# Kernel optimization log

Measured on AMD Instinct MI355X. Metric: run time of the kernel, lower is better.

## Reference

```python
import jax, jax.numpy as jnp
import numpy as np
import math

# dims: batch, seq_len, d_model, heads, head_dim
B, L, DM, H, DH = 1, 4096, 1024, 16, 64
BS, W, MAXD, DFF = 64, 16, 256, 4096  # block_size, band width (blocks), max rel distance, ffn dim
NB = L // BS


def _static_layout():
    # Static block-sparse causal band layout: tgt block n attends to src blocks [n-W+1 .. n].
    # Mirrors construct_blocksparse_rel_ids: rel = tgt_pos - src_pos, pos ids start at 1
    # (0 reserved for padding), clamp rel<-1 -> -1, rel>max_distance -> max_distance, then +1.
    n = np.arange(NB)[:, None, None, None]
    w = np.arange(W)[None, :, None, None]
    i = np.arange(BS)[None, None, :, None]
    j = np.arange(BS)[None, None, None, :]
    src_blk = n - (W - 1) + w
    # valid: block exists; diagonal block (w==W-1) is causal within-block (j<=i)
    valid = (src_blk >= 0) & ((w < W - 1) | (j <= i))
    tgt_pos = n * BS + i + 1
    src_pos = np.clip(src_blk, 0, None) * BS + j + 1
    rel = np.clip(tgt_pos - src_pos, -1, MAXD) + 1
    rel = np.where(valid, rel, 0)  # masked positions get rel id 0 (as in masked_fill_)
    src_idx = np.clip(np.arange(NB)[:, None] - (W - 1) + np.arange(W)[None, :], 0, None)
    return jnp.asarray(rel), jnp.asarray(valid), jnp.asarray(src_idx)

REL_IDS, VALID, SRC_IDX = _static_layout()  # [NB,W,BS,BS], [NB,W,BS,BS], [NB,W]


def _ln(x, g, b):
    m = x.mean(-1, keepdims=True)
    v = ((x - m) ** 2).mean(-1, keepdims=True)
    return (x - m) * jax.lax.rsqrt(v + 1e-5) * g + b


def setup_inputs() -> dict:
    key = jax.random.key(0)
    ks = jax.random.split(key, 10)
    p = lambda k, shape: jax.random.normal(k, shape, jnp.float32) * 0.02
    return dict(
        x=jax.random.normal(ks[0], (B, L, DM), jnp.float32),
        Wq=p(ks[1], (DM, DM)), Wk=p(ks[2], (DM, DM)), Wv=p(ks[3], (DM, DM)),
        Wo=p(ks[4], (DM, DM)),
        rel_emb=p(ks[5], (MAXD + 2, H)),  # per-head relative position bias table
        ln1_g=jnp.ones((DM,), jnp.float32), ln1_b=jnp.zeros((DM,), jnp.float32),
        ln2_g=jnp.ones((DM,), jnp.float32), ln2_b=jnp.zeros((DM,), jnp.float32),
        W1=p(ks[6], (DM, DFF)), b1=jnp.zeros((DFF,), jnp.float32),
        W2=p(ks[7], (DFF, DM)), b2=jnp.zeros((DM,), jnp.float32),
    )


def reference(x, Wq, Wk, Wv, Wo, rel_emb, ln1_g, ln1_b, ln2_g, ln2_b, W1, b1, W2, b2):
    h = _ln(x, ln1_g, ln1_b)

    def heads(Wt):
        return (h @ Wt).reshape(B, NB, BS, H, DH).transpose(0, 3, 1, 2, 4)  # [B,H,NB,BS,DH]

    q, k, v = heads(Wq), heads(Wk), heads(Wv)
    k_band = k[:, :, SRC_IDX]  # gather nonzero src blocks -> [B,H,NB,W,BS,DH]
    v_band = v[:, :, SRC_IDX]
    scores = jnp.einsum('bhnid,bhnwjd->bhniwj', q, k_band) / math.sqrt(DH)
    # relative position bias, per block pair and head
    bias = rel_emb[REL_IDS].transpose(4, 0, 2, 1, 3)  # [H,NB,BS,W,BS]
    scores = scores + bias[None]
    mask = VALID.transpose(0, 2, 1, 3)  # [NB,BS,W,BS]
    scores = jnp.where(mask, scores, jnp.float32(-1e30))
    p = jax.nn.softmax(scores.reshape(B, H, NB, BS, W * BS), axis=-1)
    p = p.reshape(B, H, NB, BS, W, BS)
    o = jnp.einsum('bhniwj,bhnwjd->bhnid', p, v_band)
    o = o.transpose(0, 2, 3, 1, 4).reshape(B, L, DM) @ Wo
    x = x + o
    h2 = _ln(x, ln2_g, ln2_b)
    x = x + (jax.nn.gelu(h2 @ W1 + b1) @ W2 + b2)
    return x
```

## Files before the change

kernel.cpp:

```cpp
#include <hip/hip_runtime.h>
#include <math.h>

typedef __bf16 bf16x8 __attribute__((ext_vector_type(8)));
typedef short  s16x4  __attribute__((ext_vector_type(4)));
typedef float  f32x4  __attribute__((ext_vector_type(4)));
typedef short  s16x8  __attribute__((ext_vector_type(8)));

__device__ __forceinline__ unsigned short f2bf(float f) {
    unsigned int u = __float_as_uint(f);
    u += 0x7fffu + ((u >> 16) & 1u);
    return (unsigned short)(u >> 16);
}

__device__ __forceinline__ unsigned cvt_pk_bf16(float a, float b) {
    unsigned r;
    asm volatile("v_cvt_pk_bf16_f32 %0, %1, %2" : "=v"(r) : "v"(a), "v"(b));
    return r;
}

__device__ __forceinline__ f32x4 mfma16(s16x4 a, s16x4 b, f32x4 c) {
#if __has_builtin(__builtin_amdgcn_mfma_f32_16x16x16bf16_1k)
    return __builtin_amdgcn_mfma_f32_16x16x16bf16_1k(a, b, c, 0, 0, 0);
#else
    asm volatile("s_nop 3\n\t"
                 "v_mfma_f32_16x16x16_bf16 %0, %1, %2, %0\n\t"
                 "s_nop 7\n\t"
                 "s_nop 7"
                 : "+v"(c) : "v"(a), "v"(b));
    return c;
#endif
}

__device__ __forceinline__ float gelu_tanh(float x) {
    float x3 = x * x * x;
    float t = tanhf(0.7978845608028654f * (x + 0.044715f * x3));
    return 0.5f * x * (1.0f + t);
}

__global__ __launch_bounds__(256) void tcvt4_kernel(const float* __restrict__ p0,
                                                    const float* __restrict__ p1,
                                                    const float* __restrict__ p2,
                                                    const float* __restrict__ p3,
                                                    unsigned short* __restrict__ out) {
    __shared__ float tile[32][33];
    int z = blockIdx.z;
    const float* in = (z == 0) ? p0 : (z == 1) ? p1 : (z == 2) ? p2 : p3;
    unsigned short* o = out + (size_t)z * 1048576;
    int tx = threadIdx.x, ty = threadIdx.y;
    int k0 = blockIdx.y * 32, n0 = blockIdx.x * 32;
#pragma unroll
    for (int s = 0; s < 4; ++s)
        tile[ty + s * 8][tx] = in[(size_t)(k0 + ty + s * 8) * 1024 + n0 + tx];
    __syncthreads();
#pragma unroll
    for (int s = 0; s < 4; ++s)
        o[(size_t)(n0 + ty + s * 8) * 1024 + k0 + tx] = f2bf(tile[tx][ty + s * 8]);
}

__global__ __launch_bounds__(256) void tcvt_kernel(const float* __restrict__ in,
                                                   unsigned short* __restrict__ out,
                                                   int K, int N) {
    __shared__ float tile[32][33];
    int tx = threadIdx.x, ty = threadIdx.y;
    int k0 = blockIdx.y * 32, n0 = blockIdx.x * 32;
#pragma unroll
    for (int s = 0; s < 4; ++s)
        tile[ty + s * 8][tx] = in[(size_t)(k0 + ty + s * 8) * N + n0 + tx];
    __syncthreads();
#pragma unroll
    for (int s = 0; s < 4; ++s)
        out[(size_t)(n0 + ty + s * 8) * K + k0 + tx] = f2bf(tile[tx][ty + s * 8]);
}

__global__ __launch_bounds__(256) void ln_kernel(const float* __restrict__ x,
                                                 const float* __restrict__ g,
                                                 const float* __restrict__ b,
                                                 unsigned short* __restrict__ out) {
    int row = blockIdx.x;
    int tid = threadIdx.x;
    float4 v = ((const float4*)(x + (size_t)row * 1024))[tid];
    float s  = v.x + v.y + v.z + v.w;
    float ss = v.x * v.x + v.y * v.y + v.z * v.z + v.w * v.w;
#pragma unroll
    for (int o = 32; o > 0; o >>= 1) { s += __shfl_down(s, o); ss += __shfl_down(ss, o); }
    __shared__ float red[8];
    if ((tid & 63) == 0) { red[(tid >> 6) * 2] = s; red[(tid >> 6) * 2 + 1] = ss; }
    __syncthreads();
    s  = red[0] + red[2] + red[4] + red[6];
    ss = red[1] + red[3] + red[5] + red[7];
    float mean = s * (1.0f / 1024.0f);
    float var  = ss * (1.0f / 1024.0f) - mean * mean;
    float rs   = rsqrtf(var + 1e-5f);
    float4 gv = ((const float4*)g)[tid];
    float4 bv = ((const float4*)b)[tid];
    ushort4 o4;
    o4.x = f2bf((v.x - mean) * rs * gv.x + bv.x);
    o4.y = f2bf((v.y - mean) * rs * gv.y + bv.y);
    o4.z = f2bf((v.z - mean) * rs * gv.z + bv.z);
    o4.w = f2bf((v.w - mean) * rs * gv.w + bv.w);
    ((ushort4*)(out + (size_t)row * 1024))[tid] = o4;
}

__global__ __launch_bounds__(256) void reduceln_kernel(const unsigned short* __restrict__ part,
                                                       const float* __restrict__ xin,
                                                       const float* __restrict__ g,
                                                       const float* __restrict__ b,
                                                       float* __restrict__ x2,
                                                       unsigned short* __restrict__ outbf) {
    int row = blockIdx.x;
    int tid = threadIdx.x;
    int i4  = row * 256 + tid;
    float4 r = ((const float4*)xin)[i4];
    float v0 = r.x, v1 = r.y, v2 = r.z, v3 = r.w;
#pragma unroll
    for (int sl = 0; sl < 4; ++sl) {
        ushort4 u = ((const ushort4*)(part + (size_t)sl * 4194304))[i4];
        v0 += __uint_as_float((unsigned)u.x << 16);
        v1 += __uint_as_float((unsigned)u.y << 16);
        v2 += __uint_as_float((unsigned)u.z << 16);
        v3 += __uint_as_float((unsigned)u.w << 16);
    }
    float4 o; o.x = v0; o.y = v1; o.z = v2; o.w = v3;
    ((float4*)x2)[i4] = o;

    float s  = v0 + v1 + v2 + v3;
    float ss = v0 * v0 + v1 * v1 + v2 * v2 + v3 * v3;
#pragma unroll
    for (int off = 32; off > 0; off >>= 1) { s += __shfl_down(s, off); ss += __shfl_down(ss, off); }
    __shared__ float red[8];
    if ((tid & 63) == 0) { red[(tid >> 6) * 2] = s; red[(tid >> 6) * 2 + 1] = ss; }
    __syncthreads();
    s  = red[0] + red[2] + red[4] + red[6];
    ss = red[1] + red[3] + red[5] + red[7];
    float mean = s * (1.0f / 1024.0f);
    float var  = ss * (1.0f / 1024.0f) - mean * mean;
    float rs   = rsqrtf(var + 1e-5f);
    float4 gv = ((const float4*)g)[tid];
    float4 bv = ((const float4*)b)[tid];
    ushort4 o4;
    o4.x = f2bf((v0 - mean) * rs * gv.x + bv.x);
    o4.y = f2bf((v1 - mean) * rs * gv.y + bv.y);
    o4.z = f2bf((v2 - mean) * rs * gv.z + bv.z);
    o4.w = f2bf((v3 - mean) * rs * gv.w + bv.w);
    ((ushort4*)(outbf + (size_t)row * 1024))[tid] = o4;
}

__global__ __launch_bounds__(256) void tvt_kernel(const unsigned short* __restrict__ in,
                                                  unsigned short* __restrict__ out) {
    __shared__ unsigned short tile[64][72];
    int t = threadIdx.x;
    int l0 = blockIdx.x * 64, c0 = blockIdx.y * 64;
    int tr = t >> 3, tc = (t & 7) * 8;
#pragma unroll
    for (int s = 0; s < 2; ++s) {
        int r = tr + s * 32;
        s16x8 v = *(const s16x8*)(in + (size_t)(l0 + r) * 3072 + 2048 + c0 + tc);
        *(s16x8*)(&tile[r][tc]) = v;
    }
    __syncthreads();
#pragma unroll
    for (int s = 0; s < 2; ++s) {
        int c = tr + s * 32;
        s16x8 w;
#pragma unroll
        for (int e = 0; e < 8; ++e) w[e] = (short)tile[tc + e][c];
        *(s16x8*)(out + (size_t)(c0 + c) * 4096 + l0 + tc) = w;
    }
}

__device__ __forceinline__ void stage8(const unsigned short* __restrict__ src_row0, int ld,
                                       unsigned short* ldsdst, int lane) {
    const int r8 = lane >> 3;
    const int c  = (lane & 7) ^ r8;
    const unsigned short* src = src_row0 + (size_t)r8 * ld + c * 8;
    __builtin_amdgcn_global_load_lds((const __attribute__((address_space(1))) void*)src,
                                     (__attribute__((address_space(3))) void*)ldsdst, 16, 0, 0);
}

__device__ __forceinline__ void stage64(const unsigned short* __restrict__ mat, int ld,
                                        int grow0, int kcol,
                                        unsigned short* lds_tile, int q, int wave, int lane) {
    const int l8 = lane >> 3;
    const int sc = ((lane & 7) ^ l8) << 3;
    const unsigned short* src = mat + (size_t)(grow0 + q * 64 + wave * 8 + l8) * ld + kcol + sc;
    unsigned short* dst = lds_tile + ((q * 64 + wave * 8) << 6);
    __builtin_amdgcn_global_load_lds((const __attribute__((address_space(1))) void*)src,
                                     (__attribute__((address_space(3))) void*)dst, 16, 0, 0);
}

__device__ __forceinline__ bf16x8 ldfrag(const unsigned short* tile, int row, int chunk) {
    return *(const bf16x8*)(tile + (row << 6) + (((chunk ^ row) & 7) << 3));
}

__device__ __forceinline__ s16x4 ldfrag64(const unsigned short* tile, int row, int ch16, int half) {
    return *(const s16x4*)(tile + (row << 6) + (((ch16 ^ row) & 7) << 3) + (half << 2));
}

template <int EPI>
__global__ __launch_bounds__(512, 2) void gemm256_kernel(
        const unsigned short* __restrict__ A, int lda,
        const unsigned short* __restrict__ Bt, int ldb,
        void* __restrict__ Cv, const float* __restrict__ bias,
        int ldc, int NT, int gm, int gn, unsigned long long slab_stride) {
    extern __shared__ unsigned short lds[];
    unsigned short* sA = lds;
    unsigned short* sB = lds + 2 * 256 * 64;

    const int tid  = threadIdx.x;
    const int wave = tid >> 6, lane = tid & 63;
    const int wr = wave >> 2, wc = wave & 3;
    const int lg = lane >> 4, l15 = lane & 15;

    const int nwg = gridDim.x;
    const int bid = blockIdx.x;
    const int q8 = nwg >> 3, r8 = nwg & 7;
    const int xcd = bid & 7, loc = bid >> 3;
    const int swz = (xcd < r8 ? xcd * (q8 + 1) : r8 * (q8 + 1) + (xcd - r8) * q8) + loc;
    const int split = swz / (gm * gn);
    const int rem   = swz % (gm * gn);
    const int band = rem / (gm * 4);
    const int r2   = rem % (gm * 4);
    const int brow = (r2 >> 2) << 8;
    const int bcol = (band * 4 + (r2 & 3)) << 8;
    const int kbase = split * (NT << 6);

    f32x4 acc[8][4] = {};

#define STAGE_A(tt, q_, pbuf) stage64(A, lda, brow, kbase + ((tt) << 6), sA + (pbuf) * 16384, (q_), wave, lane)
#define STAGE_B(tt, q_, pbuf) stage64(Bt, ldb, bcol, kbase + ((tt) << 6), sB + (pbuf) * 16384, (q_), wave, lane)

    STAGE_A(0, 0, 0); STAGE_A(0, 1, 0); STAGE_A(0, 2, 0); STAGE_A(0, 3, 0);
    STAGE_B(0, 0, 0); STAGE_B(0, 1, 0); STAGE_B(0, 2, 0); STAGE_B(0, 3, 0);
    STAGE_A(1, 0, 1); STAGE_A(1, 1, 1); STAGE_A(1, 2, 1); STAGE_A(1, 3, 1);
    STAGE_B(1, 0, 1); STAGE_B(1, 1, 1);
    asm volatile("s_waitcnt vmcnt(6)" ::: "memory");
    __builtin_amdgcn_s_barrier();

    for (int t = 0; t < NT; ++t) {
        const int p = t & 1;
        const unsigned short* tA = sA + p * 16384;
        const unsigned short* tB = sB + p * 16384;
        bf16x8 a0[4][2], a1[4][2], b0[2][2], b1[2][2];

#pragma unroll
        for (int im = 0; im < 4; ++im)
#pragma unroll
            for (int kk = 0; kk < 2; ++kk)
                a0[im][kk] = ldfrag(tA, wr * 128 + im * 16 + l15, lg + kk * 4);
#pragma unroll
        for (int in = 0; in < 2; ++in)
#pragma unroll
            for (int kk = 0; kk < 2; ++kk)
                b0[in][kk] = ldfrag(tB, wc * 64 + in * 16 + l15, lg + kk * 4);
        if (t + 1 < NT) { STAGE_B(t + 1, 2, p ^ 1); STAGE_B(t + 1, 3, p ^ 1); }
        __builtin_amdgcn_s_barrier();
        asm volatile("s_waitcnt lgkmcnt(0)" ::: "memory");
        __builtin_amdgcn_sched_barrier(0);
        __builtin_amdgcn_s_setprio(1);
#pragma unroll
        for (int kk = 0; kk < 2; ++kk)
#pragma unroll
            for (int im = 0; im < 4; ++im)
#pragma unroll
                for (int in = 0; in < 2; ++in)
                    acc[im][in] = __builtin_amdgcn_mfma_f32_16x16x32_bf16(a0[im][kk], b0[in][kk], acc[im][in], 0, 0, 0);
        __builtin_amdgcn_s_setprio(0);
        __builtin_amdgcn_s_barrier();

#pragma unroll
        for (int im = 0; im < 4; ++im)
#pragma unroll
            for (int kk = 0; kk < 2; ++kk)
                a1[im][kk] = ldfrag(tA, wr * 128 + 64 + im * 16 + l15, lg + kk * 4);
        if (t + 2 < NT) { STAGE_A(t + 2, 0, p); STAGE_A(t + 2, 2, p); }
        __builtin_amdgcn_s_barrier();
        asm volatile("s_waitcnt lgkmcnt(0)" ::: "memory");
        __builtin_amdgcn_sched_barrier(0);
        __builtin_amdgcn_s_setprio(1);
#pragma unroll
        for (int kk = 0; kk < 2; ++kk)
#pragma unroll
            for (int im = 0; im < 4; ++im)
#pragma unroll
                for (int in = 0; in < 2; ++in)
                    acc[4 + im][in] = __builtin_amdgcn_mfma_f32_16x16x32_bf16(a1[im][kk], b0[in][kk], acc[4 + im][in], 0, 0, 0);
        __builtin_amdgcn_s_setprio(0);
        __builtin_amdgcn_s_barrier();

#pragma unroll
        for (int in = 0; in < 2; ++in)
#pragma unroll
            for (int kk = 0; kk < 2; ++kk)
                b1[in][kk] = ldfrag(tB, wc * 64 + 32 + in * 16 + l15, lg + kk * 4);
        if (t + 2 < NT) { STAGE_A(t + 2, 1, p); STAGE_A(t + 2, 3, p); }
        __builtin_amdgcn_s_barrier();
        asm volatile("s_waitcnt lgkmcnt(0)" ::: "memory");
        __builtin_amdgcn_sched_barrier(0);
        __builtin_amdgcn_s_setprio(1);
#pragma unroll
        for (int kk = 0; kk < 2; ++kk)
#pragma unroll
            for (int im = 0; im < 4; ++im)
#pragma unroll
                for (int in = 0; in < 2; ++in)
                    acc[4 + im][2 + in] = __builtin_amdgcn_mfma_f32_16x16x32_bf16(a1[im][kk], b1[in][kk], acc[4 + im][2 + in], 0, 0, 0);
        __builtin_amdgcn_s_setprio(0);
        __builtin_amdgcn_s_barrier();

        if (t + 2 < NT) { STAGE_B(t + 2, 0, p); STAGE_B(t + 2, 1, p); }
        __builtin_amdgcn_s_barrier();
        asm volatile("s_waitcnt lgkmcnt(0)" ::: "memory");
        __builtin_amdgcn_sched_barrier(0);
        __builtin_amdgcn_s_setprio(1);
#pragma unroll
        for (int kk = 0; kk < 2; ++kk)
#pragma unroll
            for (int im = 0; im < 4; ++im)
#pragma unroll
                for (int in = 0; in < 2; ++in)
                    acc[im][2 + in] = __builtin_amdgcn_mfma_f32_16x16x32_bf16(a0[im][kk], b1[in][kk], acc[im][2 + in], 0, 0, 0);
        __builtin_amdgcn_s_setprio(0);
        if (t + 2 < NT) asm volatile("s_waitcnt vmcnt(6)" ::: "memory");
        else            asm volatile("s_waitcnt vmcnt(0)" ::: "memory");
        __builtin_amdgcn_s_barrier();
    }
#undef STAGE_A
#undef STAGE_B

#pragma unroll
    for (int mi = 0; mi < 8; ++mi)
#pragma unroll
        for (int ni = 0; ni < 4; ++ni)
#pragma unroll
            for (int rr = 0; rr < 4; ++rr) {
                int row = brow + wr * 128 + mi * 16 + lg * 4 + rr;
                int col = bcol + wc * 64 + ni * 16 + l15;
                float v = acc[mi][ni][rr];
                if (EPI == 0) {
                    ((unsigned short*)Cv)[(size_t)row * ldc + col] = f2bf(v);
                } else if (EPI == 2) {
                    v += bias[col];
                    ((unsigned short*)Cv)[(size_t)row * ldc + col] = f2bf(gelu_tanh(v));
                } else {
                    ((unsigned short*)Cv)[slab_stride * split + (size_t)row * ldc + col] = f2bf(v);
                }
            }
}

__global__ __launch_bounds__(256) void reduce4_kernel(const unsigned short* __restrict__ part,
                                                      const float* __restrict__ bias,
                                                      const float* __restrict__ resid,
                                                      float* __restrict__ out) {
    int i4 = blockIdx.x * 256 + threadIdx.x;
    float4 r  = ((const float4*)resid)[i4];
    float4 bb = ((const float4*)bias)[i4 & 255];
    float s0 = r.x + bb.x, s1 = r.y + bb.y, s2 = r.z + bb.z, s3 = r.w + bb.w;
#pragma unroll
    for (int s = 0; s < 4; ++s) {
        ushort4 u = ((const ushort4*)(part + (size_t)s * 4194304))[i4];
        s0 += __uint_as_float((unsigned)u.x << 16);
        s1 += __uint_as_float((unsigned)u.y << 16);
        s2 += __uint_as_float((unsigned)u.z << 16);
        s3 += __uint_as_float((unsigned)u.w << 16);
    }
    float4 o; o.x = s0; o.y = s1; o.z = s2; o.w = s3;
    ((float4*)out)[i4] = o;
}

__global__ __launch_bounds__(256, 4) void attn4_kernel(const unsigned short* __restrict__ qkv,
                                                       const unsigned short* __restrict__ vt,
                                                       const float* __restrict__ rel_emb,
                                                       unsigned short* __restrict__ outp) {
    const int lid = blockIdx.y * gridDim.x + blockIdx.x;
    const int rid = (lid & 7) * 128 + (lid >> 3);
    const int h   = rid >> 6;
    const int n   = rid & 63;

    const int tid  = threadIdx.x;
    const int wv   = tid >> 6;
    const int lane = tid & 63;
    const int lg   = lane >> 4;
    const int l15  = lane & 15;
    const int iq   = wv * 16 + l15;
    const int q0   = n * 64 + wv * 16;

    __shared__ __align__(16) unsigned short sK[2][4096];
    __shared__ __align__(16) unsigned short sV[2][4096];
    __shared__ float sRelF[258];

    bf16x8 qf[2];
    {
        const unsigned short* qrow = qkv + (size_t)(q0 + l15) * 3072 + h * 64 + lg * 8;
        qf[0] = *(const bf16x8*)(qrow);
        qf[1] = *(const bf16x8*)(qrow + 32);
    }

    for (int i = tid; i < 258; i += 256) sRelF[i] = rel_emb[i * 16 + h];
    const float relC = rel_emb[257 * 16 + h];

    const int tlo = (n >= 15) ? 0 : (15 - n);
    {
        const int src = n - 15 + tlo;
#pragma unroll
        for (int s = 0; s < 2; ++s) {
            int r0 = wv * 16 + s * 8;
            stage8(qkv + (size_t)(src * 64 + r0) * 3072 + 1024 + h * 64, 3072, &sK[0][r0 * 64], lane);
            stage8(vt + (size_t)(h * 64 + r0) * 4096 + src * 64, 4096, &sV[0][r0 * 64], lane);
        }
    }
    asm volatile("s_waitcnt lgkmcnt(0)" ::: "memory");
    __builtin_amdgcn_s_barrier();

    f32x4 oacc[4] = {};
    float mrow = -3e38f, lrow = 0.f;

    for (int t = tlo; t < 16; ++t) {
        const int cur = (t - tlo) & 1;
        if (t < 15) {
            const int src = n - 15 + (t + 1);
#pragma unroll
            for (int s = 0; s < 2; ++s) {
                int r0 = wv * 16 + s * 8;
                stage8(qkv + (size_t)(src * 64 + r0) * 3072 + 1024 + h * 64, 3072, &sK[cur ^ 1][r0 * 64], lane);
                stage8(vt + (size_t)(h * 64 + r0) * 4096 + src * 64, 4096, &sV[cur ^ 1][r0 * 64], lane);
            }
            asm volatile("s_waitcnt vmcnt(4)" ::: "memory");
        } else {
            asm volatile("s_waitcnt vmcnt(0)" ::: "memory");
        }
        __builtin_amdgcn_s_barrier();

        const unsigned short* tK = &sK[cur][0];
        const unsigned short* tV = &sV[cur][0];
        const int woff = 15 - t;

        f32x4 st[4] = {};
        __builtin_amdgcn_s_setprio(1);
#pragma unroll
        for (int jt = 0; jt < 4; ++jt) {
            bf16x8 kf0 = ldfrag(tK, jt * 16 + l15, lg);
            bf16x8 kf1 = ldfrag(tK, jt * 16 + l15, lg + 4);
            st[jt] = __builtin_amdgcn_mfma_f32_16x16x32_bf16(kf0, qf[0], st[jt], 0, 0, 0);
            st[jt] = __builtin_amdgcn_mfma_f32_16x16x32_bf16(kf1, qf[1], st[jt], 0, 0, 0);
        }
        __builtin_amdgcn_s_setprio(0);

        float pm = -3e38f;
        if (woff >= 5) {
#pragma unroll
            for (int jt = 0; jt < 4; ++jt)
#pragma unroll
                for (int rr = 0; rr < 4; ++rr) {
                    float v = st[jt][rr] * 0.125f + relC;
                    st[jt][rr] = v;
                    pm = fmaxf(pm, v);
                }
        } else if (woff > 0) {
#pragma unroll
            for (int jt = 0; jt < 4; ++jt)
#pragma unroll
                for (int rr = 0; rr < 4; ++rr) {
                    int j = jt * 16 + lg * 4 + rr;
                    int relid = min(woff * 64 + iq - j, 256) + 1;
                    float v = st[jt][rr] * 0.125f + sRelF[relid];
                    st[jt][rr] = v;
                    pm = fmaxf(pm, v);
                }
        } else {
#pragma unroll
            for (int jt = 0; jt < 4; ++jt)
#pragma unroll
                for (int rr = 0; rr < 4; ++rr) {
                    int j = jt * 16 + lg * 4 + rr;
                    float v = (j <= iq) ? (st[jt][rr] * 0.125f + sRelF[iq - j + 1]) : -1e30f;
                    st[jt][rr] = v;
                    pm = fmaxf(pm, v);
                }
        }
        pm = fmaxf(pm, __shfl_xor(pm, 16));
        pm = fmaxf(pm, __shfl_xor(pm, 32));
        float mn  = fmaxf(mrow, pm);
        float scl = __expf(mrow - mn);
        mrow = mn;

        float rs = 0.f;
        unsigned pk0[4], pk1[4];
#pragma unroll
        for (int jt = 0; jt < 4; ++jt) {
            float p0 = __expf(st[jt][0] - mn);
            float p1 = __expf(st[jt][1] - mn);
            float p2 = __expf(st[jt][2] - mn);
            float p3 = __expf(st[jt][3] - mn);
            rs += (p0 + p1) + (p2 + p3);
            pk0[jt] = cvt_pk_bf16(p0, p1);
            pk1[jt] = cvt_pk_bf16(p2, p3);
        }
        rs += __shfl_xor(rs, 16);
        rs += __shfl_xor(rs, 32);
        lrow = lrow * scl + rs;
#pragma unroll
        for (int dt = 0; dt < 4; ++dt)
#pragma unroll
            for (int rr = 0; rr < 4; ++rr)
                oacc[dt][rr] *= scl;

        __builtin_amdgcn_s_setprio(1);
#pragma unroll
        for (int ks = 0; ks < 4; ++ks) {
            union { unsigned u[2]; s16x4 v; } pu;
            pu.u[0] = pk0[ks]; pu.u[1] = pk1[ks];
#pragma unroll
            for (int dt = 0; dt < 4; ++dt) {
                s16x4 vf = ldfrag64(tV, dt * 16 + l15, 2 * ks + (lg >> 1), lg & 1);
                oacc[dt] = mfma16(vf, pu.v, oacc[dt]);
            }
        }
        __builtin_amdgcn_s_setprio(0);
        __builtin_amdgcn_s_barrier();
    }

    float inv = 1.0f / lrow;
    unsigned short* sO = &sK[0][0] + wv * 1024;
#pragma unroll
    for (int dt = 0; dt < 4; ++dt)
#pragma unroll
        for (int c = 0; c < 2; ++c) {
            unsigned pr = cvt_pk_bf16(oacc[dt][2 * c] * inv, oacc[dt][2 * c + 1] * inv);
            int d  = dt * 16 + lg * 4 + 2 * c;
            int off = (l15 << 6) + ((((d >> 3) ^ (l15 & 7)) & 7) << 3) + (d & 7);
            *(unsigned*)(sO + off) = pr;
        }
#pragma unroll
    for (int c2 = 0; c2 < 2; ++c2) {
        int ch = lg + 4 * c2;
        bf16x8 ov = ldfrag(sO, l15, ch);
        *(s16x8*)(outp + (size_t)(q0 + l15) * 1024 + h * 64 + ch * 8) = *(const s16x8*)&ov;
    }
}

extern "C" void kernel_launch(void* const* d_in, const int* in_sizes, int n_in,
                              void* d_out, int out_size, void* d_ws, size_t ws_size,
                              hipStream_t stream) {
    const float* x    = (const float*)d_in[0];
    const float* Wq   = (const float*)d_in[1];
    const float* Wk   = (const float*)d_in[2];
    const float* Wv   = (const float*)d_in[3];
    const float* Wo   = (const float*)d_in[4];
    const float* rel  = (const float*)d_in[5];
    const float* ln1g = (const float*)d_in[6];
    const float* ln1b = (const float*)d_in[7];
    const float* ln2g = (const float*)d_in[8];
    const float* ln2b = (const float*)d_in[9];
    const float* W1   = (const float*)d_in[10];
    const float* b1   = (const float*)d_in[11];
    const float* W2   = (const float*)d_in[12];
    const float* b2   = (const float*)d_in[13];

    char* ws = (char*)d_ws;
    unsigned short* wqkvT  = (unsigned short*)(ws + 0);
    unsigned short* woT    = wqkvT + 3145728;
    unsigned short* attnb  = (unsigned short*)(ws + 8388608);
    unsigned short* w1T    = (unsigned short*)(ws + 16777216);
    unsigned short* hbuf   = (unsigned short*)(ws + 25165824);
    unsigned short* w2T    = (unsigned short*)(ws + 33554432);
    float*          x2     = (float*)(ws + 41943040);
    unsigned short* qkv    = (unsigned short*)(ws + 58720256);
    unsigned short* vt     = (unsigned short*)(ws + 83886080);
    unsigned short* wopart = (unsigned short*)(ws + 58720256);
    unsigned short* gbuf   = (unsigned short*)(ws + 58720256);
    unsigned short* part   = (unsigned short*)(ws + 0);

    const int smem = 131072;
    hipFuncSetAttribute((const void*)gemm256_kernel<0>, hipFuncAttributeMaxDynamicSharedMemorySize, smem);
    hipFuncSetAttribute((const void*)gemm256_kernel<2>, hipFuncAttributeMaxDynamicSharedMemorySize, smem);
    hipFuncSetAttribute((const void*)gemm256_kernel<4>, hipFuncAttributeMaxDynamicSharedMemorySize, smem);

    dim3 tb(32, 8);
    tcvt4_kernel<<<dim3(32, 32, 4), tb, 0, stream>>>(Wq, Wk, Wv, Wo, wqkvT);
    tcvt_kernel<<<dim3(128, 32), tb, 0, stream>>>(W1, w1T, 1024, 4096);
    tcvt_kernel<<<dim3(32, 128), tb, 0, stream>>>(W2, w2T, 4096, 1024);

    ln_kernel<<<4096, 256, 0, stream>>>(x, ln1g, ln1b, hbuf);

    gemm256_kernel<0><<<192, 512, smem, stream>>>(hbuf, 1024, wqkvT, 1024, qkv,
                                                  nullptr, 3072, 16, 16, 12, 0ULL);

    tvt_kernel<<<dim3(64, 16), 256, 0, stream>>>(qkv, vt);

    attn4_kernel<<<dim3(64, 16), 256, 0, stream>>>(qkv, vt, rel, attnb);

    gemm256_kernel<4><<<256, 512, smem, stream>>>(attnb, 1024, woT, 1024, wopart,
                                                  nullptr, 1024, 4, 16, 4, 4194304ULL);
    reduceln_kernel<<<4096, 256, 0, stream>>>(wopart, x, ln2g, ln2b, x2, hbuf);

    gemm256_kernel<2><<<256, 512, smem, stream>>>(hbuf, 1024, w1T, 1024, gbuf,
                                                  b1, 4096, 16, 16, 16, 0ULL);

    gemm256_kernel<4><<<256, 512, smem, stream>>>(gbuf, 4096, w2T, 4096, part,
                                                  nullptr, 1024, 16, 16, 4, 4194304ULL);

    reduce4_kernel<<<4096, 256, 0, stream>>>(part, b2, x2, (float*)d_out);
}
```

Baseline: 235.7 us.

## Software-pipeline LDS fragment reads across GEMM phases and simplify GELU

Restructures the 256x256 GEMM main loop so LDS fragment reads for the next phase, and for the next k-tile, are issued with inline ds_read_b128 before the current MFMA block. Partial lgkmcnt waits replace full drains, and the number of barriers per iteration drops. The B tile for stage 1 is fully prefetched in the prologue and the global-to-LDS staging order is reshuffled. GELU tanh is rewritten as x*sigmoid(2z) using __expf, which is cheaper but approximate. The risks are hand-tuned waitcnt correctness and higher register pressure from keeping more fragments live.

```diff
diff --git a/kernel.cpp b/kernel.cpp
--- a/kernel.cpp
+++ b/kernel.cpp
@@ -32,9 +32,8 @@
 }
 
 __device__ __forceinline__ float gelu_tanh(float x) {
-    float x3 = x * x * x;
-    float t = tanhf(0.7978845608028654f * (x + 0.044715f * x3));
-    return 0.5f * x * (1.0f + t);
+    float z = 1.5957691216057308f * (x + 0.044715f * x * x * x);
+    return x / (1.0f + __expf(-z));
 }
 
 __global__ __launch_bounds__(256) void tcvt4_kernel(const float* __restrict__ p0,
@@ -196,6 +195,15 @@
     return *(const s16x4*)(tile + (row << 6) + (((ch16 ^ row) & 7) << 3) + (half << 2));
 }
 
+__device__ __forceinline__ unsigned lds_byte(unsigned base, int row, int chunk) {
+    return base + (row << 7) + (((chunk ^ row) & 7) << 4);
+}
+__device__ __forceinline__ bf16x8 ds_frag(unsigned addr) {
+    bf16x8 r;
+    asm volatile("ds_read_b128 %0, %1" : "=v"(r) : "v"(addr));
+    return r;
+}
+
 template <int EPI>
 __global__ __launch_bounds__(512, 2) void gemm256_kernel(
         const unsigned short* __restrict__ A, int lda,
@@ -210,6 +218,9 @@
     const int wave = tid >> 6, lane = tid & 63;
     const int wr = wave >> 2, wc = wave & 3;
     const int lg = lane >> 4, l15 = lane & 15;
+
+    const unsigned uA = (unsigned)(size_t)(__attribute__((address_space(3))) void*)sA;
+    const unsigned uB = (unsigned)(size_t)(__attribute__((address_space(3))) void*)sB;
 
     const int nwg = gridDim.x;
     const int bid = blockIdx.x;
@@ -225,6 +236,7 @@
     const int kbase = split * (NT << 6);
 
     f32x4 acc[8][4] = {};
+    bf16x8 a0[4][2], a1[4][2], b0[2][2], b1[2][2];
 
 #define STAGE_A(tt, q_, pbuf) stage64(A, lda, brow, kbase + ((tt) << 6), sA + (pbuf) * 16384, (q_), wave, lane)
 #define STAGE_B(tt, q_, pbuf) stage64(Bt, ldb, bcol, kbase + ((tt) << 6), sB + (pbuf) * 16384, (q_), wave, lane)
@@ -232,30 +244,35 @@
     STAGE_A(0, 0, 0); STAGE_A(0, 1, 0); STAGE_A(0, 2, 0); STAGE_A(0, 3, 0);
     STAGE_B(0, 0, 0); STAGE_B(0, 1, 0); STAGE_B(0, 2, 0); STAGE_B(0, 3, 0);
     STAGE_A(1, 0, 1); STAGE_A(1, 1, 1); STAGE_A(1, 2, 1); STAGE_A(1, 3, 1);
-    STAGE_B(1, 0, 1); STAGE_B(1, 1, 1);
-    asm volatile("s_waitcnt vmcnt(6)" ::: "memory");
+    STAGE_B(1, 0, 1); STAGE_B(1, 1, 1); STAGE_B(1, 2, 1); STAGE_B(1, 3, 1);
+    asm volatile("s_waitcnt vmcnt(8)" ::: "memory");
+    __builtin_amdgcn_sched_barrier(0);
     __builtin_amdgcn_s_barrier();
+#pragma unroll
+    for (int im = 0; im < 4; ++im)
+#pragma unroll
+        for (int kk = 0; kk < 2; ++kk)
+            a0[im][kk] = ds_frag(lds_byte(uA, wr * 128 + im * 16 + l15, lg + kk * 4));
+#pragma unroll
+    for (int in = 0; in < 2; ++in)
+#pragma unroll
+        for (int kk = 0; kk < 2; ++kk)
+            b0[in][kk] = ds_frag(lds_byte(uB, wc * 64 + in * 16 + l15, lg + kk * 4));
 
     for (int t = 0; t < NT; ++t) {
         const int p = t & 1;
-        const unsigned short* tA = sA + p * 16384;
-        const unsigned short* tB = sB + p * 16384;
-        bf16x8 a0[4][2], a1[4][2], b0[2][2], b1[2][2];
+        const unsigned uAp = uA + p * 32768, uBp = uB + p * 32768;
+        const unsigned uAn = uA + (p ^ 1) * 32768, uBn = uB + (p ^ 1) * 32768;
 
 #pragma unroll
         for (int im = 0; im < 4; ++im)
 #pragma unroll
             for (int kk = 0; kk < 2; ++kk)
-                a0[im][kk] = ldfrag(tA, wr * 128 + im * 16 + l15, lg + kk * 4);
-#pragma unroll
-        for (int in = 0; in < 2; ++in)
-#pragma unroll
-            for (int kk = 0; kk < 2; ++kk)
-                b0[in][kk] = ldfrag(tB, wc * 64 + in * 16 + l15, lg + kk * 4);
-        if (t + 1 < NT) { STAGE_B(t + 1, 2, p ^ 1); STAGE_B(t + 1, 3, p ^ 1); }
+                a1[im][kk] = ds_frag(lds_byte(uAp, wr * 128 + 64 + im * 16 + l15, lg + kk * 4));
+        asm volatile("s_waitcnt lgkmcnt(8)" ::: "memory");
+        __builtin_amdgcn_sched_barrier(0);
         __builtin_amdgcn_s_barrier();
-        asm volatile("s_waitcnt lgkmcnt(0)" ::: "memory");
-        __builtin_amdgcn_sched_barrier(0);
+        if (t + 2 < NT) { STAGE_A(t + 2, 0, p); STAGE_A(t + 2, 2, p); }
         __builtin_amdgcn_s_setprio(1);
 #pragma unroll
         for (int kk = 0; kk < 2; ++kk)
@@ -265,17 +282,16 @@
                 for (int in = 0; in < 2; ++in)
                     acc[im][in] = __builtin_amdgcn_mfma_f32_16x16x32_bf16(a0[im][kk], b0[in][kk], acc[im][in], 0, 0, 0);
         __builtin_amdgcn_s_setprio(0);
+
+#pragma unroll
+        for (int in = 0; in < 2; ++in)
+#pragma unroll
+            for (int kk = 0; kk < 2; ++kk)
+                b1[in][kk] = ds_frag(lds_byte(uBp, wc * 64 + 32 + in * 16 + l15, lg + kk * 4));
+        asm volatile("s_waitcnt lgkmcnt(4)" ::: "memory");
+        __builtin_amdgcn_sched_barrier(0);
         __builtin_amdgcn_s_barrier();
-
-#pragma unroll
-        for (int im = 0; im < 4; ++im)
-#pragma unroll
-            for (int kk = 0; kk < 2; ++kk)
-                a1[im][kk] = ldfrag(tA, wr * 128 + 64 + im * 16 + l15, lg + kk * 4);
-        if (t + 2 < NT) { STAGE_A(t + 2, 0, p); STAGE_A(t + 2, 2, p); }
-        __builtin_amdgcn_s_barrier();
-        asm volatile("s_waitcnt lgkmcnt(0)" ::: "memory");
-        __builtin_amdgcn_sched_barrier(0);
+        if (t + 2 < NT) { STAGE_A(t + 2, 1, p); STAGE_A(t + 2, 3, p); }
         __builtin_amdgcn_s_setprio(1);
 #pragma unroll
         for (int kk = 0; kk < 2; ++kk)
@@ -285,17 +301,40 @@
                 for (int in = 0; in < 2; ++in)
                     acc[4 + im][in] = __builtin_amdgcn_mfma_f32_16x16x32_bf16(a1[im][kk], b0[in][kk], acc[4 + im][in], 0, 0, 0);
         __builtin_amdgcn_s_setprio(0);
-        __builtin_amdgcn_s_barrier();
-
-#pragma unroll
-        for (int in = 0; in < 2; ++in)
-#pragma unroll
-            for (int kk = 0; kk < 2; ++kk)
-                b1[in][kk] = ldfrag(tB, wc * 64 + 32 + in * 16 + l15, lg + kk * 4);
-        if (t + 2 < NT) { STAGE_A(t + 2, 1, p); STAGE_A(t + 2, 3, p); }
-        __builtin_amdgcn_s_barrier();
+
         asm volatile("s_waitcnt lgkmcnt(0)" ::: "memory");
         __builtin_amdgcn_sched_barrier(0);
+        __builtin_amdgcn_s_barrier();
+        if (t + 2 < NT) { STAGE_B(t + 2, 0, p); STAGE_B(t + 2, 1, p); }
+        __builtin_amdgcn_s_setprio(1);
+#pragma unroll
+        for (int kk = 0; kk < 2; ++kk)
+#pragma unroll
+            for (int im = 0; im < 4; ++im)
+#pragma unroll
+                for (int in = 0; in < 2; ++in)
+                    acc[im][2 + in] = __builtin_amdgcn_mfma_f32_16x16x32_bf16(a0[im][kk], b1[in][kk], acc[im][2 + in], 0, 0, 0);
+        __builtin_amdgcn_s_setprio(0);
+
+        if (t + 1 < NT) {
+            if (t + 2 < NT) asm volatile("s_waitcnt vmcnt(6)" ::: "memory");
+            else            asm volatile("s_waitcnt vmcnt(0)" ::: "memory");
+            __builtin_amdgcn_sched_barrier(0);
+        }
+        __builtin_amdgcn_s_barrier();
+        if (t + 2 < NT) { STAGE_B(t + 2, 2, p); STAGE_B(t + 2, 3, p); }
+        if (t + 1 < NT) {
+#pragma unroll
+            for (int im = 0; im < 4; ++im)
+#pragma unroll
+                for (int kk = 0; kk < 2; ++kk)
+                    a0[im][kk] = ds_frag(lds_byte(uAn, wr * 128 + im * 16 + l15, lg + kk * 4));
+#pragma unroll
+            for (int in = 0; in < 2; ++in)
+#pragma unroll
+                for (int kk = 0; kk < 2; ++kk)
+                    b0[in][kk] = ds_frag(lds_byte(uBn, wc * 64 + in * 16 + l15, lg + kk * 4));
+        }
         __builtin_amdgcn_s_setprio(1);
 #pragma unroll
         for (int kk = 0; kk < 2; ++kk)
@@ -305,24 +344,6 @@
                 for (int in = 0; in < 2; ++in)
                     acc[4 + im][2 + in] = __builtin_amdgcn_mfma_f32_16x16x32_bf16(a1[im][kk], b1[in][kk], acc[4 + im][2 + in], 0, 0, 0);
         __builtin_amdgcn_s_setprio(0);
-        __builtin_amdgcn_s_barrier();
-
-        if (t + 2 < NT) { STAGE_B(t + 2, 0, p); STAGE_B(t + 2, 1, p); }
-        __builtin_amdgcn_s_barrier();
-        asm volatile("s_waitcnt lgkmcnt(0)" ::: "memory");
-        __builtin_amdgcn_sched_barrier(0);
-        __builtin_amdgcn_s_setprio(1);
-#pragma unroll
-        for (int kk = 0; kk < 2; ++kk)
-#pragma unroll
-            for (int im = 0; im < 4; ++im)
-#pragma unroll
-                for (int in = 0; in < 2; ++in)
-                    acc[im][2 + in] = __builtin_amdgcn_mfma_f32_16x16x32_bf16(a0[im][kk], b1[in][kk], acc[im][2 + in], 0, 0, 0);
-        __builtin_amdgcn_s_setprio(0);
-        if (t + 2 < NT) asm volatile("s_waitcnt vmcnt(6)" ::: "memory");
-        else            asm volatile("s_waitcnt vmcnt(0)" ::: "memory");
-        __builtin_amdgcn_s_barrier();
     }
 #undef STAGE_A
 #undef STAGE_B
```

New measurement: 227.2 us. 3.6% less time.
